# Optimization experiments

Measured on AMD Instinct MI355X. Metric: run time of the kernel, lower is better.

The kernel has to match this reference:

```python
import jax, jax.numpy as jnp
import numpy as np

# config mirroring init_kwargs
PPD = (64, 64)                      # points_per_dim (spatial grid)
GRID_RANGE = ((-1.0, 1.0), (-1.0, 1.0))
B, N, NT, DX, DZ = 2, 2048, 8, 3, 16
INIT_LS = 0.1
TIME_DIM = 0


def construct_grid():
    axes = [jnp.linspace(lo, hi, p, dtype=jnp.float32) for (lo, hi), p in zip(GRID_RANGE, PPD)]
    mesh = jnp.meshgrid(*axes, indexing='ij')
    return jnp.stack(mesh, axis=-1)  # (H, W, 2)


def setup_inputs() -> dict:
    key = jax.random.key(0)
    k1, k2, k3 = jax.random.split(key, 3)
    x = jax.random.uniform(k1, (B, N, DX), jnp.float32, -1.0, 1.0)
    z = jax.random.normal(k2, (B, N, DZ), jnp.float32)
    time_grid = jnp.sort(jax.random.uniform(k3, (B, NT), jnp.float32, -1.0, 1.0), axis=-1)
    # raw parameter s.t. softplus(param) == INIT_LS (inverse-softplus init)
    lengthscale_param = jnp.full((DX,), float(np.log(np.exp(INIT_LS) - 1.0)), jnp.float32)
    return {"x": x, "z": z, "time_grid": time_grid, "lengthscale_param": lengthscale_param}


def reference(x, z, time_grid, lengthscale_param):
    H, W = PPD
    b = x.shape[0]
    t = time_grid.shape[1]
    grid = construct_grid()  # (H, W, 2)

    ls = 1e-5 + jax.nn.softplus(lengthscale_param)  # (DX,)

    # x_grid: [b, t, H, W, DX] with the time coordinate at coord index TIME_DIM(=0)
    spatial = jnp.broadcast_to(grid, (b, t, H, W, 2))
    tg = jnp.broadcast_to(time_grid[:, :, None, None, None], (b, t, H, W, 1))
    x_grid = jnp.concatenate([tg, spatial], axis=-1)

    G = t * H * W
    xg_flat = x_grid.reshape(b, G, DX)

    # pre_exp[b, g, n] = sum_d (xg - x)^2 / ls_d^2, computed via scaled-coordinate
    # norm expansion to avoid materializing the [b, G, n, DX] difference tensor.
    a = xg_flat / ls                          # [b, G, DX]
    c = x / ls                                # [b, n, DX]
    pre_exp = (jnp.sum(a * a, axis=-1)[:, :, None]
               + jnp.sum(c * c, axis=-1)[:, None, :]
               - 2.0 * jnp.einsum('bgd,bnd->bgn', a, c))
    weights = jnp.exp(-0.5 * pre_exp)         # [b, G, n]  (RBF weights)

    z_grid = jnp.einsum('bgn,bne->bge', weights, z)  # [b, G, DZ]
    z_grid = z_grid.reshape(b, t, H, W, DZ)
    return x_grid, z_grid
```

## Files before the change

### kernel.cpp

```cpp
#include <hip/hip_runtime.h>
#include <math.h>

#define B_  2
#define N_  2048
#define NT_ 8
#define DZ_ 16
#define H_  64
#define W_  64

#define XGRID_SIZE (B_*NT_*H_*W_*3)
#define CUT 16.0f
#define CH  64
#define RSH 72

using half8   = __attribute__((ext_vector_type(8))) _Float16;
using half2v  = __attribute__((ext_vector_type(2))) _Float16;
using floatx4 = __attribute__((ext_vector_type(4))) float;

__global__ __launch_bounds__(256, 4) void fused_kernel(
    const float* __restrict__ x,
    const float* __restrict__ z,
    const float* __restrict__ tg,
    const float* __restrict__ lsp,
    float* __restrict__ out)
{
    const int i    = blockIdx.x & 63;
    const int t    = (blockIdx.x >> 6) & 7;
    const int b    = blockIdx.x >> 9;
    const int tid  = threadIdx.x;
    const int w    = tid >> 6;
    const int lane = tid & 63;
    const int quad = lane >> 4;
    const int col  = lane & 15;

    const float step = 2.0f / 63.0f;
    const float C    = 0.84932180f;

    const float r0 = C / (1e-5f + log1pf(expf(lsp[0])));
    const float r1 = C / (1e-5f + log1pf(expf(lsp[1])));
    const float r2 = C / (1e-5f + log1pf(expf(lsp[2])));

    const float tval = tg[b*NT_ + t];
    const float gi   = -1.0f + step * (float)i;

    __shared__ float2    cuc[N_ + CH];
    __shared__ int       cidx[N_ + CH];
    __shared__ _Float16  zT[2][16 * RSH];
    __shared__ int s_cnt;

    if (tid == 0) s_cnt = 0;
    __syncthreads();

    const float* __restrict__ xb = x + b*N_*3;
    for (int k0 = 0; k0 < N_; k0 += 256) {
        int k = k0 + tid;
        float x0 = xb[k*3 + 0];
        float x1 = xb[k*3 + 1];
        float x2 = xb[k*3 + 2];
        float dt = (tval - x0) * r0;
        float di = (gi   - x1) * r1;
        float sq = fmaf(dt, dt, di*di);
        bool keep = (sq < CUT);
        unsigned long long mb = __ballot(keep);
        int cnt = __popcll(mb);
        int base = 0;
        if (lane == 0) base = atomicAdd(&s_cnt, cnt);
        base = __shfl(base, 0, 64);
        if (keep) {
            int rank = __popcll(mb & ((1ull << lane) - 1ull));
            int pos  = base + rank;
            cuc[pos]  = make_float2(sq, x2 * r2);
            cidx[pos] = k;
        }
    }

    if (tid < 192) {
        int jj = tid / 3;
        int c  = tid - jj*3;
        float gj = -1.0f + step * (float)jj;
        float v  = (c == 0) ? tval : ((c == 1) ? gi : gj);
        out[(size_t)blockIdx.x * 192 + tid] = v;
    }

    __syncthreads();
    const int M = s_cnt;
    if (tid < CH) {
        cuc[M + tid]  = make_float2(1e9f, 0.f);
        cidx[M + tid] = 0;
    }
    __syncthreads();

    const int NC = (M + CH - 1) / CH;

    const float* __restrict__ zb = z + b*N_*DZ_;
    const float ajm = (-1.0f + step * (float)(w*16 + col)) * r2;

    const int se = tid & 15;
    const int ks = (tid >> 4) * 4;

    floatx4 acc = {0.f, 0.f, 0.f, 0.f};
    float rg0, rg1, rg2, rg3;

    if (NC > 0) {
        rg0 = zb[(size_t)cidx[ks + 0] * DZ_ + se];
        rg1 = zb[(size_t)cidx[ks + 1] * DZ_ + se];
        rg2 = zb[(size_t)cidx[ks + 2] * DZ_ + se];
        rg3 = zb[(size_t)cidx[ks + 3] * DZ_ + se];
    }

    for (int c = 0; c < NC; ++c) {
        const int buf = c & 1;

        half2v h01 = { (_Float16)rg0, (_Float16)rg1 };
        half2v h23 = { (_Float16)rg2, (_Float16)rg3 };
        *(half2v*)&zT[buf][se*RSH + ks]     = h01;
        *(half2v*)&zT[buf][se*RSH + ks + 2] = h23;
        __syncthreads();

        if (c + 1 < NC) {
            const int base2 = (c + 1) * CH;
            rg0 = zb[(size_t)cidx[base2 + ks + 0] * DZ_ + se];
            rg1 = zb[(size_t)cidx[base2 + ks + 1] * DZ_ + se];
            rg2 = zb[(size_t)cidx[base2 + ks + 2] * DZ_ + se];
            rg3 = zb[(size_t)cidx[base2 + ks + 3] * DZ_ + se];
        }

        const int base = c * CH;
        const float2* __restrict__ mp0 = &cuc[base + quad*8];
        const float2* __restrict__ mp1 = &cuc[base + 32 + quad*8];

        half8 a0, a1;
        #pragma unroll
        for (int jj = 0; jj < 8; ++jj) {
            float2 mm = mp0[jj];
            float d = ajm - mm.y;
            a0[jj] = (_Float16)exp2f(-fmaf(d, d, mm.x));
        }
        #pragma unroll
        for (int jj = 0; jj < 8; ++jj) {
            float2 mm = mp1[jj];
            float d = ajm - mm.y;
            a1[jj] = (_Float16)exp2f(-fmaf(d, d, mm.x));
        }

        half8 b0 = *(const half8*)&zT[buf][col*RSH + quad*8];
        half8 b1 = *(const half8*)&zT[buf][col*RSH + 32 + quad*8];

        acc = __builtin_amdgcn_mfma_f32_16x16x32_f16(a0, b0, acc, 0, 0, 0);
        acc = __builtin_amdgcn_mfma_f32_16x16x32_f16(a1, b1, acc, 0, 0, 0);
    }

    float* og = out + XGRID_SIZE + (size_t)blockIdx.x * (W_ * DZ_);
    #pragma unroll
    for (int reg = 0; reg < 4; ++reg) {
        int j = w*16 + quad*4 + reg;
        og[j*DZ_ + col] = acc[reg];
    }
}

extern "C" void kernel_launch(void* const* d_in, const int* in_sizes, int n_in,
                              void* d_out, int out_size, void* d_ws, size_t ws_size,
                              hipStream_t stream) {
    const float* x   = (const float*)d_in[0];
    const float* z   = (const float*)d_in[1];
    const float* tg  = (const float*)d_in[2];
    const float* lsp = (const float*)d_in[3];

    float* out = (float*)d_out;

    fused_kernel<<<1024, 256, 0, stream>>>(x, z, tg, lsp, out);
}
```

Measured before the change: 75.80 us.

## Split candidate K dimension across waves with register-direct B operands and LDS reduction

Instead of giving each wave 16 output columns over all candidates, each wave now covers all 64 columns for its own 32-candidate slice of a 128-wide chunk. It loads z values straight into registers as the MFMA B operand, which removes the shared-memory transpose and the per-chunk barrier. The per-wave partial sums are then reduced through shared memory aliased over the candidate buffer. The cutoff is also lowered from 16 to 12, which drops more distant points, lowers cost, and slightly changes accuracy.

Result: faster. 72.76 us (-4.0%).

```diff
diff --git a/kernel.cpp b/kernel.cpp
--- a/kernel.cpp
+++ b/kernel.cpp
@@ -9,12 +9,10 @@
 #define W_  64
 
 #define XGRID_SIZE (B_*NT_*H_*W_*3)
-#define CUT 16.0f
-#define CH  64
-#define RSH 72
+#define CUT 12.0f
+#define CH  128
 
 using half8   = __attribute__((ext_vector_type(8))) _Float16;
-using half2v  = __attribute__((ext_vector_type(2))) _Float16;
 using floatx4 = __attribute__((ext_vector_type(4))) float;
 
 __global__ __launch_bounds__(256, 4) void fused_kernel(
@@ -43,10 +41,13 @@
     const float tval = tg[b*NT_ + t];
     const float gi   = -1.0f + step * (float)i;
 
-    __shared__ float2    cuc[N_ + CH];
-    __shared__ int       cidx[N_ + CH];
-    __shared__ _Float16  zT[2][16 * RSH];
-    __shared__ int s_cnt;
+    union REDU {
+        float2 cuc[N_ + CH];
+        float  red[4][64][DZ_ + 1];
+    };
+    __shared__ REDU sm;
+    __shared__ int  cidx[N_ + CH];
+    __shared__ int  s_cnt;
 
     if (tid == 0) s_cnt = 0;
     __syncthreads();
@@ -69,8 +70,8 @@
         if (keep) {
             int rank = __popcll(mb & ((1ull << lane) - 1ull));
             int pos  = base + rank;
-            cuc[pos]  = make_float2(sq, x2 * r2);
-            cidx[pos] = k;
+            sm.cuc[pos] = make_float2(sq, x2 * r2);
+            cidx[pos]   = k;
         }
     }
 
@@ -85,77 +86,101 @@
     __syncthreads();
     const int M = s_cnt;
     if (tid < CH) {
-        cuc[M + tid]  = make_float2(1e9f, 0.f);
-        cidx[M + tid] = 0;
+        sm.cuc[M + tid] = make_float2(1e9f, 0.f);
+        cidx[M + tid]   = 0;
     }
     __syncthreads();
 
     const int NC = (M + CH - 1) / CH;
 
     const float* __restrict__ zb = z + b*N_*DZ_;
-    const float ajm = (-1.0f + step * (float)(w*16 + col)) * r2;
+    const int koff = w*32 + (quad << 3);
 
-    const int se = tid & 15;
-    const int ks = (tid >> 4) * 4;
+    const float aj0 = (-1.0f + step * (float)( 0 + col)) * r2;
+    const float aj1 = (-1.0f + step * (float)(16 + col)) * r2;
+    const float aj2 = (-1.0f + step * (float)(32 + col)) * r2;
+    const float aj3 = (-1.0f + step * (float)(48 + col)) * r2;
 
-    floatx4 acc = {0.f, 0.f, 0.f, 0.f};
-    float rg0, rg1, rg2, rg3;
+    floatx4 acc0 = {0.f,0.f,0.f,0.f};
+    floatx4 acc1 = {0.f,0.f,0.f,0.f};
+    floatx4 acc2 = {0.f,0.f,0.f,0.f};
+    floatx4 acc3 = {0.f,0.f,0.f,0.f};
 
-    if (NC > 0) {
-        rg0 = zb[(size_t)cidx[ks + 0] * DZ_ + se];
-        rg1 = zb[(size_t)cidx[ks + 1] * DZ_ + se];
-        rg2 = zb[(size_t)cidx[ks + 2] * DZ_ + se];
-        rg3 = zb[(size_t)cidx[ks + 3] * DZ_ + se];
+    float zreg[8];
+    {
+        int idx[8];
+        #pragma unroll
+        for (int jj = 0; jj < 8; ++jj) idx[jj] = cidx[koff + jj];
+        #pragma unroll
+        for (int jj = 0; jj < 8; ++jj)
+            zreg[jj] = zb[(size_t)idx[jj] * DZ_ + col];
     }
 
     for (int c = 0; c < NC; ++c) {
-        const int buf = c & 1;
+        half8 bf;
+        #pragma unroll
+        for (int jj = 0; jj < 8; ++jj) bf[jj] = (_Float16)zreg[jj];
 
-        half2v h01 = { (_Float16)rg0, (_Float16)rg1 };
-        half2v h23 = { (_Float16)rg2, (_Float16)rg3 };
-        *(half2v*)&zT[buf][se*RSH + ks]     = h01;
-        *(half2v*)&zT[buf][se*RSH + ks + 2] = h23;
-        __syncthreads();
+        const int base = c*CH + koff;
+        float2 mm[8];
+        #pragma unroll
+        for (int jj = 0; jj < 8; ++jj) mm[jj] = sm.cuc[base + jj];
 
         if (c + 1 < NC) {
-            const int base2 = (c + 1) * CH;
-            rg0 = zb[(size_t)cidx[base2 + ks + 0] * DZ_ + se];
-            rg1 = zb[(size_t)cidx[base2 + ks + 1] * DZ_ + se];
-            rg2 = zb[(size_t)cidx[base2 + ks + 2] * DZ_ + se];
-            rg3 = zb[(size_t)cidx[base2 + ks + 3] * DZ_ + se];
+            const int base2 = (c + 1)*CH + koff;
+            int idx[8];
+            #pragma unroll
+            for (int jj = 0; jj < 8; ++jj) idx[jj] = cidx[base2 + jj];
+            #pragma unroll
+            for (int jj = 0; jj < 8; ++jj)
+                zreg[jj] = zb[(size_t)idx[jj] * DZ_ + col];
         }
 
-        const int base = c * CH;
-        const float2* __restrict__ mp0 = &cuc[base + quad*8];
-        const float2* __restrict__ mp1 = &cuc[base + 32 + quad*8];
-
-        half8 a0, a1;
+        half8 a0, a1, a2, a3;
         #pragma unroll
         for (int jj = 0; jj < 8; ++jj) {
-            float2 mm = mp0[jj];
-            float d = ajm - mm.y;
-            a0[jj] = (_Float16)exp2f(-fmaf(d, d, mm.x));
-        }
-        #pragma unroll
-        for (int jj = 0; jj < 8; ++jj) {
-            float2 mm = mp1[jj];
-            float d = ajm - mm.y;
-            a1[jj] = (_Float16)exp2f(-fmaf(d, d, mm.x));
+            float s  = mm[jj].x;
+            float cx = mm[jj].y;
+            float d0 = aj0 - cx;
+            float d1 = aj1 - cx;
+            float d2 = aj2 - cx;
+            float d3 = aj3 - cx;
+            a0[jj] = (_Float16)exp2f(-fmaf(d0, d0, s));
+            a1[jj] = (_Float16)exp2f(-fmaf(d1, d1, s));
+            a2[jj] = (_Float16)exp2f(-fmaf(d2, d2, s));
+            a3[jj] = (_Float16)exp2f(-fmaf(d3, d3, s));
         }
 
-        half8 b0 = *(const half8*)&zT[buf][col*RSH + quad*8];
-        half8 b1 = *(const half8*)&zT[buf][col*RSH + 32 + quad*8];
-
-        acc = __builtin_amdgcn_mfma_f32_16x16x32_f16(a0, b0, acc, 0, 0, 0);
-        acc = __builtin_amdgcn_mfma_f32_16x16x32_f16(a1, b1, acc, 0, 0, 0);
+        acc0 = __builtin_amdgcn_mfma_f32_16x16x32_f16(a0, bf, acc0, 0, 0, 0);
+        acc1 = __builtin_amdgcn_mfma_f32_16x16x32_f16(a1, bf, acc1, 0, 0, 0);
+        acc2 = __builtin_amdgcn_mfma_f32_16x16x32_f16(a2, bf, acc2, 0, 0, 0);
+        acc3 = __builtin_amdgcn_mfma_f32_16x16x32_f16(a3, bf, acc3, 0, 0, 0);
     }
 
+    __syncthreads();
+
+    #pragma unroll
+    for (int r = 0; r < 4; ++r) sm.red[w][ 0 + quad*4 + r][col] = acc0[r];
+    #pragma unroll
+    for (int r = 0; r < 4; ++r) sm.red[w][16 + quad*4 + r][col] = acc1[r];
+    #pragma unroll
+    for (int r = 0; r < 4; ++r) sm.red[w][32 + quad*4 + r][col] = acc2[r];
+    #pragma unroll
+    for (int r = 0; r < 4; ++r) sm.red[w][48 + quad*4 + r][col] = acc3[r];
+    __syncthreads();
+
+    const int jj = tid >> 2;
+    const int eg = (tid & 3) * 4;
+    float4 s4 = make_float4(0.f, 0.f, 0.f, 0.f);
+    #pragma unroll
+    for (int ww = 0; ww < 4; ++ww) {
+        s4.x += sm.red[ww][jj][eg + 0];
+        s4.y += sm.red[ww][jj][eg + 1];
+        s4.z += sm.red[ww][jj][eg + 2];
+        s4.w += sm.red[ww][jj][eg + 3];
+    }
     float* og = out + XGRID_SIZE + (size_t)blockIdx.x * (W_ * DZ_);
-    #pragma unroll
-    for (int reg = 0; reg < 4; ++reg) {
-        int j = w*16 + quad*4 + reg;
-        og[j*DZ_ + col] = acc[reg];
-    }
+    *(float4*)(og + jj*DZ_ + eg) = s4;
 }
 
 extern "C" void kernel_launch(void* const* d_in, const int* in_sizes, int n_in,
```
